# Kernel optimization log

Measured on AMD Instinct MI355X. Metric: run time of the kernel, lower is better.

The kernel has to match this reference:

```python
import jax, jax.numpy as jnp
import numpy as np
import math

PRE_D = 2048   # pre_d_model (scaled from 8192)
D = 4096       # d_model (scaled from 16384)
N = 64         # d_state (scaled from 128)
K = 4          # d_conv
EXP = 2
L = 128        # sequence_length
DI1 = EXP * PRE_D
DI2 = EXP * D
DTR1 = math.ceil(PRE_D / 16)
DTR2 = math.ceil(D / 16)


def _sinusoid(max_len, d):
    pe = np.zeros((max_len, d), np.float32)
    pos = np.arange(max_len, dtype=np.float32)[:, None]
    div = np.exp(np.arange(0, d, 2, dtype=np.float32) * (-math.log(10000.0) / d))
    pe[:, 0::2] = np.sin(pos * div)
    pe[:, 1::2] = np.cos(pos * div)
    return jnp.asarray(pe)


def _mamba_params(key, d_in, d_out, di, dtr, n, k):
    ks = jax.random.split(key, 6)
    s = 0.02
    dt = jnp.exp(jax.random.uniform(ks[4], (di,)) * (math.log(0.1) - math.log(1e-3)) + math.log(1e-3))
    return dict(
        in_proj=jax.random.normal(ks[0], (2 * di, d_in)) * s,
        conv_w=jax.random.normal(ks[1], (di, k)) * s,
        conv_b=jnp.zeros((di,)),
        x_proj=jax.random.normal(ks[2], (dtr + 2 * n, di)) * s,
        dt_w=jax.random.normal(ks[3], (di, dtr)) * s,
        dt_b=jnp.log(jnp.expm1(dt)),  # softplus^-1 of dt init
        A_log=jnp.log(jnp.tile(jnp.arange(1, n + 1, dtype=jnp.float32), (di, 1))),
        D=jnp.ones((di,)),
        out_proj=jax.random.normal(ks[5], (d_out, di)) * s,
    )


def setup_inputs() -> dict:
    key = jax.random.key(0)
    k1, k2, k3, k4 = jax.random.split(key, 4)
    inp = {
        'pe': _sinusoid(L, PRE_D),                              # (L, PRE_D)
        'to_cond_w': jax.random.normal(k3, (PRE_D, 1)) * 0.02,  # Linear(1 -> PRE_D)
        'to_cond_b': jnp.zeros((PRE_D,)),
        'condition': jax.random.normal(k4, (1,)),
        'batch': 1,
    }
    for pref, p in (('m1_', _mamba_params(k1, PRE_D, PRE_D, DI1, DTR1, N, K)),
                    ('m2_', _mamba_params(k2, PRE_D, D, DI2, DTR2, N, K))):
        for name, v in p.items():
            inp[pref + name] = v
    return inp


def _silu(x):
    return x * jax.nn.sigmoid(x)


def _mamba(x, in_w, cw, cb, xp_w, dt_w, dt_b, A_log, Dp, out_w, dtr, n):
    # x: (B, L, d_in)
    xz = x @ in_w.T                     # (B, L, 2*di)
    xr, z = jnp.split(xz, 2, axis=-1)
    kk = cw.shape[1]
    Lx = xr.shape[1]
    xpad = jnp.pad(xr, ((0, 0), (kk - 1, 0), (0, 0)))  # causal pad
    conv = sum(cw[:, i] * xpad[:, i:i + Lx, :] for i in range(kk)) + cb
    xr = _silu(conv)
    dbc = xr @ xp_w.T                   # (B, L, dtr + 2n)
    dt = dbc[..., :dtr]
    Bm = dbc[..., dtr:dtr + n]
    Cm = dbc[..., dtr + n:]
    dt = jax.nn.softplus(dt @ dt_w.T + dt_b)           # (B, L, di)
    A = -jnp.exp(A_log)                                 # (di, n)
    dA = jnp.exp(jnp.einsum('bld,dn->bldn', dt, A))
    dBx = jnp.einsum('bld,bln,bld->bldn', dt, Bm, xr)

    def comb(c1, c2):
        a1, b1 = c1
        a2, b2 = c2
        return a2 * a1, a2 * b1 + b2

    _, h = jax.lax.associative_scan(comb, (dA, dBx), axis=1)  # (B, L, di, n)
    y = jnp.einsum('bldn,bln->bld', h, Cm) + xr * Dp
    y = y * _silu(z)
    return y @ out_w.T


def reference(pe, to_cond_w, to_cond_b, condition,
              m1_in_proj, m1_conv_w, m1_conv_b, m1_x_proj, m1_dt_w, m1_dt_b, m1_A_log, m1_D, m1_out_proj,
              m2_in_proj, m2_conv_w, m2_conv_b, m2_x_proj, m2_dt_w, m2_dt_b, m2_A_log, m2_D, m2_out_proj,
              batch):
    cond = condition.reshape(-1, 1, 1)
    c = jnp.einsum('bli,oi->blo', cond, to_cond_w) + to_cond_b   # (Bc,1,PRE_D)
    x = jnp.tile(pe[None], (batch, 1, 1)) + c                    # (B, L, PRE_D)
    x = _mamba(x, m1_in_proj, m1_conv_w, m1_conv_b, m1_x_proj, m1_dt_w, m1_dt_b,
               m1_A_log, m1_D, m1_out_proj, DTR1, N)
    x = _mamba(x, m2_in_proj, m2_conv_w, m2_conv_b, m2_x_proj, m2_dt_w, m2_dt_b,
               m2_A_log, m2_D, m2_out_proj, DTR2, N)
    return x
```

## Files before the change

kernel.cpp:

```cpp
#include <hip/hip_runtime.h>
#include <hip/hip_bf16.h>
#include <math.h>


typedef __attribute__((ext_vector_type(8))) short short8_t;
typedef __attribute__((ext_vector_type(4))) float f32x4;

__device__ __forceinline__ float sigmoidf_(float x) {
  return 1.0f / (1.0f + __expf(-x));
}
__device__ __forceinline__ float softplusf_(float x) {
  return fmaxf(x, 0.0f) + log1pf(expf(-fabsf(x)));
}
__device__ __forceinline__ void splitbf(float f, ushort& h, ushort& lo) {
  __hip_bfloat16 hb = __float2bfloat16(f);
  h = *reinterpret_cast<ushort*>(&hb);
  float hf = __bfloat162float(hb);
  __hip_bfloat16 lb = __float2bfloat16(f - hf);
  lo = *reinterpret_cast<ushort*>(&lb);
}
__device__ __forceinline__ void tsplit(float f, ushort& h, ushort& lo) {
  unsigned u = __float_as_uint(f);
  h = (ushort)(u >> 16);
  float r = f - __uint_as_float(u & 0xFFFF0000u);
  lo = (ushort)(__float_as_uint(r) >> 16);
}
__device__ __forceinline__ size_t poff(int l, int d) {
  return (size_t)(d >> 5) * 8192 + (size_t)((d >> 3) & 3) * 1024 +
         (size_t)l * 8 + (d & 7);
}
__device__ __forceinline__ void g2l16(const float* g, float* lp) {
  __builtin_amdgcn_global_load_lds(
      (const __attribute__((address_space(1))) unsigned int*)g,
      (__attribute__((address_space(3))) unsigned int*)lp, 16, 0, 0);
}

__global__ __launch_bounds__(256) void k_prep(const float* __restrict__ pe,
                                              const float* __restrict__ cw,
                                              const float* __restrict__ cb,
                                              const float* __restrict__ cond,
                                              ushort* __restrict__ xp) {
  int i = blockIdx.x * 256 + threadIdx.x;
  int d = i & 2047;
  int l = i >> 11;
  float v = pe[i] + cond[0] * cw[d] + cb[d];
  ushort h, lo;
  splitbf(v, h, lo);
  size_t o = poff(l, d);
  xp[o] = h;
  xp[o + 4096] = lo;
}

#define KWS 32
__global__ __launch_bounds__(256, 4) void k_gemmW(const ushort* __restrict__ Ap,
                                                  const float* __restrict__ W, int ldw,
                                                  float* __restrict__ P,
                                                  int N, int Ks) {
  __shared__ float Wlds[2][4][32][32];

  const int n0   = blockIdx.x * 128;
  const int m0   = blockIdx.y * 64;
  const int s    = blockIdx.z;
  const int kbeg = s * Ks;
  const int t    = threadIdx.x;
  const int l    = t & 63;
  const int w    = t >> 6;
  const int lr   = l & 15;
  const int lg   = l >> 4;

  f32x4 acc[4][2];
#pragma unroll
  for (int mi = 0; mi < 4; ++mi)
#pragma unroll
    for (int ni = 0; ni < 2; ++ni) acc[mi][ni] = (f32x4)(0.0f);

  const int grow = l >> 3;
  const int gg   = (l & 7) ^ (grow & 7);
  const float* gW[4];
#pragma unroll
  for (int i = 0; i < 4; ++i)
    gW[i] = W + (size_t)(n0 + 32 * w + 8 * i + grow) * ldw + kbeg + gg * 4;

  const ushort* pA0 = Ap + (size_t)(kbeg >> 5) * 8192;
  const int nIter = Ks / KWS;
  const int j0 = (blockIdx.x * 3 + blockIdx.y * 5 + s) % nIter;

#pragma unroll
  for (int i = 0; i < 4; ++i)
    g2l16(gW[i] + (size_t)j0 * KWS, &Wlds[0][w][8 * i][0]);

  for (int j = 0; j < nIter; ++j) {
    const int bi = j & 1;
    const int cur = (j0 + j) % nIter;
    const bool more = (j + 1 < nIter);

    const ushort* pAj = pA0 + (size_t)cur * 8192;
    short8_t ah[4], al[4];
#pragma unroll
    for (int mi = 0; mi < 4; ++mi) {
      const size_t fo = (size_t)lg * 1024 + (size_t)(m0 + 16 * mi + lr) * 8;
      ah[mi] = *(const short8_t*)(pAj + fo);
      al[mi] = *(const short8_t*)(pAj + 4096 + fo);
    }
    __builtin_amdgcn_sched_barrier(0);
    if (more) {
      const int nxt = (j0 + j + 1) % nIter;
#pragma unroll
      for (int i = 0; i < 4; ++i)
        g2l16(gW[i] + (size_t)nxt * KWS, &Wlds[bi ^ 1][w][8 * i][0]);
      asm volatile("s_waitcnt vmcnt(4)" ::: "memory");
    } else {
      asm volatile("s_waitcnt vmcnt(0)" ::: "memory");
    }
    __builtin_amdgcn_sched_barrier(0);
    const float* Wb = &Wlds[bi][w][0][0];
#pragma unroll
    for (int ni = 0; ni < 2; ++ni) {
      const int r32 = 16 * ni + lr;
      const int rsw = r32 & 7;
      const float4 v0 = *(const float4*)(Wb + r32 * 32 + (((2 * lg) ^ rsw) * 4));
      const float4 v1 = *(const float4*)(Wb + r32 * 32 + (((2 * lg + 1) ^ rsw) * 4));
      short8_t bh, bl;
      {
        const float f8[8] = {v0.x, v0.y, v0.z, v0.w, v1.x, v1.y, v1.z, v1.w};
#pragma unroll
        for (int e = 0; e < 8; ++e) {
          ushort h, lo;
          tsplit(f8[e], h, lo);
          bh[e] = (short)h;
          bl[e] = (short)lo;
        }
      }
#pragma unroll
      for (int mi = 0; mi < 4; ++mi) {
        acc[mi][ni] = __builtin_amdgcn_mfma_f32_16x16x32_bf16(ah[mi], bh, acc[mi][ni], 0, 0, 0);
        acc[mi][ni] = __builtin_amdgcn_mfma_f32_16x16x32_bf16(al[mi], bh, acc[mi][ni], 0, 0, 0);
        acc[mi][ni] = __builtin_amdgcn_mfma_f32_16x16x32_bf16(ah[mi], bl, acc[mi][ni], 0, 0, 0);
      }
    }
  }

  float* Pd = P + (size_t)s * 128 * N + n0 + 32 * w;
#pragma unroll
  for (int mi = 0; mi < 4; ++mi)
#pragma unroll
    for (int ni = 0; ni < 2; ++ni) {
#pragma unroll
      for (int jj = 0; jj < 4; ++jj) {
        const int m = m0 + 16 * mi + 4 * lg + jj;
        Pd[(size_t)m * N + 16 * ni + lr] = acc[mi][ni][jj];
      }
    }
}

#define KSTEP 32
__global__ __launch_bounds__(256, 2) void k_gemm(const ushort* __restrict__ Ap,
                                                 const float* __restrict__ W, int ldw,
                                                 float* __restrict__ P,
                                                 int N, int Ks) {
  __shared__ ushort Ws[2][2][4][128][8];

  const int n0   = blockIdx.x * 128;
  const int s    = blockIdx.z;
  const int kbeg = s * Ks;
  const int t    = threadIdx.x;
  const int l    = t & 63;
  const int w    = t >> 6;
  const int wm   = w >> 1;
  const int wn   = w & 1;
  const int lr   = l & 15;
  const int lg   = l >> 4;

  f32x4 acc[4][4];
#pragma unroll
  for (int mi = 0; mi < 4; ++mi)
#pragma unroll
    for (int ni = 0; ni < 4; ++ni) acc[mi][ni] = (f32x4)(0.0f);

  const int srow = t >> 3;
  const int sk16 = t & 7;
  const int skb  = sk16 >> 1;
  const int se0  = (sk16 & 1) * 4;
  const float* pWg = W + (size_t)(n0 + srow) * ldw + kbeg + sk16 * 4;

  const ushort* pAc = Ap + (size_t)(kbeg >> 5) * 8192;
  const int arow = 64 * wm + lr;
  const int brow = 64 * wn + lr;

  const int nIter = Ks / KSTEP;
  float4 wv[4];

#pragma unroll
  for (int r = 0; r < 4; ++r)
    wv[r] = *(const float4*)(pWg + (size_t)(r * 32) * ldw);
#pragma unroll
  for (int r = 0; r < 4; ++r) {
    ushort4 h4, l4;
    splitbf(wv[r].x, h4.x, l4.x); splitbf(wv[r].y, h4.y, l4.y);
    splitbf(wv[r].z, h4.z, l4.z); splitbf(wv[r].w, h4.w, l4.w);
    *(ushort4*)&Ws[0][0][skb][srow + 32 * r][se0] = h4;
    *(ushort4*)&Ws[0][1][skb][srow + 32 * r][se0] = l4;
  }
  __syncthreads();

  for (int j = 0; j < nIter; ++j) {
    const int bi = j & 1;
    const bool more = (j + 1 < nIter);

    const ushort* pAj = pAc + (size_t)j * 8192;
    short8_t ah[4], al[4];
#pragma unroll
    for (int mi = 0; mi < 4; ++mi) {
      const size_t fo = (size_t)lg * 1024 + (size_t)(arow + 16 * mi) * 8;
      ah[mi] = *(const short8_t*)(pAj + fo);
      al[mi] = *(const short8_t*)(pAj + 4096 + fo);
    }
    if (more) {
      const size_t ko = (size_t)(j + 1) * KSTEP;
#pragma unroll
      for (int r = 0; r < 4; ++r)
        wv[r] = *(const float4*)(pWg + ko + (size_t)(r * 32) * ldw);
    }
    short8_t bh[4], bl[4];
#pragma unroll
    for (int ni = 0; ni < 4; ++ni) {
      bh[ni] = *(const short8_t*)&Ws[bi][0][lg][brow + 16 * ni][0];
      bl[ni] = *(const short8_t*)&Ws[bi][1][lg][brow + 16 * ni][0];
    }
#pragma unroll
    for (int mi = 0; mi < 4; ++mi)
#pragma unroll
      for (int ni = 0; ni < 4; ++ni) {
        acc[mi][ni] = __builtin_amdgcn_mfma_f32_16x16x32_bf16(ah[mi], bh[ni], acc[mi][ni], 0, 0, 0);
        acc[mi][ni] = __builtin_amdgcn_mfma_f32_16x16x32_bf16(al[mi], bh[ni], acc[mi][ni], 0, 0, 0);
        acc[mi][ni] = __builtin_amdgcn_mfma_f32_16x16x32_bf16(ah[mi], bl[ni], acc[mi][ni], 0, 0, 0);
      }
    if (more) {
#pragma unroll
      for (int r = 0; r < 4; ++r) {
        ushort4 h4, l4;
        splitbf(wv[r].x, h4.x, l4.x); splitbf(wv[r].y, h4.y, l4.y);
        splitbf(wv[r].z, h4.z, l4.z); splitbf(wv[r].w, h4.w, l4.w);
        *(ushort4*)&Ws[bi ^ 1][0][skb][srow + 32 * r][se0] = h4;
        *(ushort4*)&Ws[bi ^ 1][1][skb][srow + 32 * r][se0] = l4;
      }
    }
    __syncthreads();
  }

  float* Pd = P + (size_t)s * 128 * N + n0 + 64 * wn;
#pragma unroll
  for (int mi = 0; mi < 4; ++mi)
#pragma unroll
    for (int ni = 0; ni < 4; ++ni) {
#pragma unroll
      for (int jj = 0; jj < 4; ++jj) {
        const int m = 64 * wm + 16 * mi + 4 * lg + jj;
        Pd[(size_t)m * N + 16 * ni + lr] = acc[mi][ni][jj];
      }
    }
}

__global__ __launch_bounds__(256) void k_reduce(const float* __restrict__ P,
                                                float* __restrict__ Y,
                                                ushort* __restrict__ Yp,
                                                int MN, int N, int S, int ep,
                                                const float* __restrict__ bias) {
  int i = (blockIdx.x * 256 + threadIdx.x) * 4;
  if (i >= MN) return;
  float4 v = *(const float4*)&P[i];
  for (int s = 1; s < S; ++s) {
    float4 p = *(const float4*)&P[(size_t)s * MN + i];
    v.x += p.x; v.y += p.y; v.z += p.z; v.w += p.w;
  }
  int n = i % N;
  int l = i / N;
  if (ep & 1) {
    const float4 b = *(const float4*)&bias[n];
    v.x = softplusf_(v.x + b.x);
    v.y = softplusf_(v.y + b.y);
    v.z = softplusf_(v.z + b.z);
    v.w = softplusf_(v.w + b.w);
  }
  if (ep & 4) *(float4*)&Y[i] = v;
  if (ep & 2) {
    ushort4 h4, l4;
    splitbf(v.x, h4.x, l4.x);
    splitbf(v.y, h4.y, l4.y);
    splitbf(v.z, h4.z, l4.z);
    splitbf(v.w, h4.w, l4.w);
    size_t o = poff(l, n);
    *(ushort4*)&Yp[o] = h4;
    *(ushort4*)&Yp[o + 4096] = l4;
  }
}

__global__ __launch_bounds__(256) void k_reduceA(const float* __restrict__ P,
                                                 float* __restrict__ Y, int MN) {
  int g = blockIdx.y;
  int i = (blockIdx.x * 256 + threadIdx.x) * 4;
  if (i >= MN) return;
  const float* Pp = P + (size_t)g * 8 * MN;
  float4 v = *(const float4*)&Pp[i];
  for (int s = 1; s < 8; ++s) {
    float4 p = *(const float4*)&Pp[(size_t)s * MN + i];
    v.x += p.x; v.y += p.y; v.z += p.z; v.w += p.w;
  }
  *(float4*)&Y[(size_t)g * MN + i] = v;
}

__global__ __launch_bounds__(256) void k_conv_silu(const float* __restrict__ xz,
                                                   const float* __restrict__ cw,
                                                   const float* __restrict__ cb,
                                                   float* __restrict__ xc,
                                                   ushort* __restrict__ xcp,
                                                   int DI, int lg2DI) {
  int i = blockIdx.x * 256 + threadIdx.x;
  int l = i >> lg2DI;
  int d = i & (DI - 1);
  const float4 w = *(const float4*)&cw[d * 4];
  const float* xr = xz + d;
  int ld = 2 * DI;
  float s = cb[d];
  s += w.w * xr[l * ld];
  if (l >= 1) s += w.z * xr[(l - 1) * ld];
  if (l >= 2) s += w.y * xr[(l - 2) * ld];
  if (l >= 3) s += w.x * xr[(l - 3) * ld];
  float v = s * sigmoidf_(s);
  xc[i] = v;
  ushort h, lo;
  splitbf(v, h, lo);
  size_t o = poff(l, d);
  xcp[o] = h;
  xcp[o + 4096] = lo;
}

__global__ __launch_bounds__(256) void k_scan(const float* __restrict__ dt,
                                              const float* __restrict__ xc,
                                              const float* __restrict__ dbc,
                                              const float* __restrict__ A_log,
                                              const float* __restrict__ Dp,
                                              float* __restrict__ y,
                                              int DI, int DTR) {
  __shared__ float cs[4][32][65];
  const int wid = threadIdx.x >> 6;
  const int n   = threadIdx.x & 63;
  const int d   = blockIdx.x * 4 + wid;
  const int du  = __builtin_amdgcn_readfirstlane(d);
  const float A  = -__expf(A_log[(size_t)du * 64 + n]);
  const float Dd = Dp[du];
  const int ldbc = DTR + 128;
  const float* Bp = dbc + DTR + n;
  const float* Cp = dbc + DTR + 64 + n;
  float h = 0.0f;
  for (int l0 = 0; l0 < 128; l0 += 32) {
#pragma unroll 8
    for (int l = l0; l < l0 + 32; ++l) {
      float dtv = dt[(size_t)l * DI + du];
      float xcv = xc[(size_t)l * DI + du];
      float dA  = __expf(dtv * A);
      float bx  = dtv * xcv;
      h = fmaf(dA, h, bx * Bp[(size_t)l * ldbc]);
      cs[wid][l - l0][n] = h * Cp[(size_t)l * ldbc];
    }
    __syncthreads();
    const int r = n & 31, hf = n >> 5;
    float ssum = 0.0f;
#pragma unroll
    for (int j = 0; j < 32; ++j) ssum += cs[wid][r][hf * 32 + j];
    ssum += __shfl_xor(ssum, 32, 64);
    if (n < 32) {
      int ll = l0 + r;
      float xcv = xc[(size_t)ll * DI + du];
      y[(size_t)ll * DI + du] = ssum + xcv * Dd;
    }
    __syncthreads();
  }
}

__global__ __launch_bounds__(256) void k_gate(const float* __restrict__ yb,
                                              const float* __restrict__ xz,
                                              ushort* __restrict__ yp,
                                              int DI, int lg2DI) {
  int i = blockIdx.x * 256 + threadIdx.x;
  int l = i >> lg2DI;
  int d = i & (DI - 1);
  float z = xz[((size_t)l << (lg2DI + 1)) + DI + d];
  float v = yb[i] * (z * sigmoidf_(z));
  ushort h, lo;
  splitbf(v, h, lo);
  size_t o = poff(l, d);
  yp[o] = h;
  yp[o + 4096] = lo;
}

struct GemmCtx {
  float* part;
  float* part2;
  long long cap;
};

static inline void reduce_stage(float* dstF, ushort* dstP, int N, int S, int ep,
                                const float* bias, const GemmCtx& cx,
                                hipStream_t stream) {
  const int MN = 128 * N;
  const int rb = (MN / 4 + 255) / 256;
  if (S <= 16) {
    k_reduce<<<rb, 256, 0, stream>>>(cx.part, dstF, dstP, MN, N, S, ep, bias);
  } else {
    k_reduceA<<<dim3(rb, S / 8), 256, 0, stream>>>(cx.part, cx.part2, MN);
    k_reduce<<<rb, 256, 0, stream>>>(cx.part2, dstF, dstP, MN, N, S / 8, ep, bias);
  }
}

static inline void gemmS(const ushort* Ap, const float* W, int ldw,
                         float* dstF, ushort* dstP,
                         int N, int K, int Sdes, int ep,
                         const float* bias, const GemmCtx& cx, hipStream_t stream) {
  int S = Sdes;
  if (S > K / KSTEP) S = K / KSTEP;
  if (S < 1) S = 1;
  while (S > 1 && (long long)S * 128 * N > cx.cap) S >>= 1;
  const int Ks = K / S;
  const bool direct = (S == 1 && ep == 4);
  dim3 g(N / 128, 1, S);
  k_gemm<<<g, 256, 0, stream>>>(Ap, W, ldw, direct ? dstF : cx.part, N, Ks);
  if (!direct) reduce_stage(dstF, dstP, N, S, ep, bias, cx, stream);
}

static inline void gemmW(const ushort* Ap, const float* W, int ldw,
                         float* dstF, ushort* dstP,
                         int N, int K, int Sdes, int ep,
                         const float* bias, const GemmCtx& cx, hipStream_t stream) {
  int S = Sdes;
  if (S > K / KWS) S = K / KWS;
  if (S < 1) S = 1;
  while (S > 1 && (long long)S * 128 * N > cx.cap) S >>= 1;
  const int Ks = K / S;
  const bool direct = (S == 1 && ep == 4);
  dim3 g(N / 128, 2, S);
  k_gemmW<<<g, 256, 0, stream>>>(Ap, W, ldw, direct ? dstF : cx.part, N, Ks);
  if (!direct) reduce_stage(dstF, dstP, N, S, ep, bias, cx, stream);
}

extern "C" void kernel_launch(void* const* d_in, const int* in_sizes, int n_in,
                              void* d_out, int out_size, void* d_ws, size_t ws_size,
                              hipStream_t stream) {
  const float* pe        = (const float*)d_in[0];
  const float* to_cond_w = (const float*)d_in[1];
  const float* to_cond_b = (const float*)d_in[2];
  const float* condition = (const float*)d_in[3];
  const int o = (in_sizes[4] == 1) ? 5 : 4;
  const float* m1_in_proj  = (const float*)d_in[o + 0];
  const float* m1_conv_w   = (const float*)d_in[o + 1];
  const float* m1_conv_b   = (const float*)d_in[o + 2];
  const float* m1_x_proj   = (const float*)d_in[o + 3];
  const float* m1_dt_w     = (const float*)d_in[o + 4];
  const float* m1_dt_b     = (const float*)d_in[o + 5];
  const float* m1_A_log    = (const float*)d_in[o + 6];
  const float* m1_D        = (const float*)d_in[o + 7];
  const float* m1_out_proj = (const float*)d_in[o + 8];
  const float* m2_in_proj  = (const float*)d_in[o + 9];
  const float* m2_conv_w   = (const float*)d_in[o + 10];
  const float* m2_conv_b   = (const float*)d_in[o + 11];
  const float* m2_x_proj   = (const float*)d_in[o + 12];
  const float* m2_dt_w     = (const float*)d_in[o + 13];
  const float* m2_dt_b     = (const float*)d_in[o + 14];
  const float* m2_A_log    = (const float*)d_in[o + 15];
  const float* m2_D        = (const float*)d_in[o + 16];
  const float* m2_out_proj = (const float*)d_in[o + 17];

  float* ws = (float*)d_ws;
  float*  xz   = ws;
  float*  xc   = ws + 2097152;
  float*  dbc  = ws + 3145728;
  float*  dtb  = ws + 3194880;
  float*  yb   = ws + 4243456;
  ushort* x0p  = (ushort*)(ws + 5292032);
  ushort* xcp  = (ushort*)(ws + 5554176);
  ushort* dbcp = (ushort*)(ws + 6602752);
  ushort* ybp  = (ushort*)(ws + 6651904);
  ushort* midp = (ushort*)(ws + 7700480);
  float*  part2 = ws + 7962624;
  float*  part  = ws + 8749056;

  GemmCtx cx;
  cx.part = part;
  cx.part2 = part2;
  cx.cap = (long long)(ws_size / 4) - 8749056;
  if (cx.cap < 0) cx.cap = 0;

  k_prep<<<1024, 256, 0, stream>>>(pe, to_cond_w, to_cond_b, condition, x0p);

  gemmW(x0p, m1_in_proj, 2048, xz, nullptr, 8192, 2048, 8, 4, nullptr, cx, stream);
  k_conv_silu<<<(128 * 4096) / 256, 256, 0, stream>>>(xz, m1_conv_w, m1_conv_b,
                                                      xc, xcp, 4096, 12);
  gemmS(xcp, m1_x_proj, 4096, dbc, dbcp, 256, 4096, 128, 6, nullptr, cx, stream);
  gemmS(dbcp, m1_dt_w, 128, dtb, nullptr, 4096, 128, 4, 5, m1_dt_b, cx, stream);
  k_scan<<<1024, 256, 0, stream>>>(dtb, xc, dbc, m1_A_log, m1_D, yb, 4096, 128);
  k_gate<<<(128 * 4096) / 256, 256, 0, stream>>>(yb, xz, ybp, 4096, 12);
  gemmW(ybp, m1_out_proj, 4096, nullptr, midp, 2048, 4096, 16, 2, nullptr, cx, stream);

  gemmW(midp, m2_in_proj, 2048, xz, nullptr, 16384, 2048, 4, 4, nullptr, cx, stream);
  k_conv_silu<<<(128 * 8192) / 256, 256, 0, stream>>>(xz, m2_conv_w, m2_conv_b,
                                                      xc, xcp, 8192, 13);
  gemmS(xcp, m2_x_proj, 8192, dbc, dbcp, 384, 8192, 128, 6, nullptr, cx, stream);
  gemmS(dbcp, m2_dt_w, 256, dtb, nullptr, 8192, 256, 4, 5, m2_dt_b, cx, stream);
  k_scan<<<2048, 256, 0, stream>>>(dtb, xc, dbc, m2_A_log, m2_D, yb, 8192, 256);
  k_gate<<<(128 * 8192) / 256, 256, 0, stream>>>(yb, xz, ybp, 8192, 13);
  gemmW(ybp, m2_out_proj, 8192, (float*)d_out, nullptr, 4096, 8192, 8, 4, nullptr, cx, stream);
}
```

Before: 372.8 us.

## Widen gemmW tile to full M, triple-buffer W and double-buffer A registers

The weight-streaming GEMM kernel now handles all 128 rows per block instead of splitting M across two blocks. This halves redundant loads of the fp32 weight tile. The W tile moves from a double to a triple LDS buffer, A fragments are double-buffered in registers across an unrolled-by-two loop, and a fixed vmcnt(20) wait keeps more loads in flight. Split-K counts are doubled to keep the grid size similar. The cost is higher register pressure (launch bounds drop from 4 to 2 waves), and the loop now assumes an even iteration count.

```diff
diff --git a/kernel.cpp b/kernel.cpp
--- a/kernel.cpp
+++ b/kernel.cpp
@@ -52,14 +52,13 @@
 }
 
 #define KWS 32
-__global__ __launch_bounds__(256, 4) void k_gemmW(const ushort* __restrict__ Ap,
+__global__ __launch_bounds__(256, 2) void k_gemmW(const ushort* __restrict__ Ap,
                                                   const float* __restrict__ W, int ldw,
                                                   float* __restrict__ P,
                                                   int N, int Ks) {
-  __shared__ float Wlds[2][4][32][32];
+  __shared__ float Wlds[3][4][32][32];
 
   const int n0   = blockIdx.x * 128;
-  const int m0   = blockIdx.y * 64;
   const int s    = blockIdx.z;
   const int kbeg = s * Ks;
   const int t    = threadIdx.x;
@@ -68,9 +67,9 @@
   const int lr   = l & 15;
   const int lg   = l >> 4;
 
-  f32x4 acc[4][2];
-#pragma unroll
-  for (int mi = 0; mi < 4; ++mi)
+  f32x4 acc[8][2];
+#pragma unroll
+  for (int mi = 0; mi < 8; ++mi)
 #pragma unroll
     for (int ni = 0; ni < 2; ++ni) acc[mi][ni] = (f32x4)(0.0f);
 
@@ -83,71 +82,87 @@
 
   const ushort* pA0 = Ap + (size_t)(kbeg >> 5) * 8192;
   const int nIter = Ks / KWS;
-  const int j0 = (blockIdx.x * 3 + blockIdx.y * 5 + s) % nIter;
-
-#pragma unroll
-  for (int i = 0; i < 4; ++i)
-    g2l16(gW[i] + (size_t)j0 * KWS, &Wlds[0][w][8 * i][0]);
-
-  for (int j = 0; j < nIter; ++j) {
-    const int bi = j & 1;
-    const int cur = (j0 + j) % nIter;
-    const bool more = (j + 1 < nIter);
-
-    const ushort* pAj = pA0 + (size_t)cur * 8192;
-    short8_t ah[4], al[4];
-#pragma unroll
-    for (int mi = 0; mi < 4; ++mi) {
-      const size_t fo = (size_t)lg * 1024 + (size_t)(m0 + 16 * mi + lr) * 8;
-      ah[mi] = *(const short8_t*)(pAj + fo);
-      al[mi] = *(const short8_t*)(pAj + 4096 + fo);
-    }
+  const int j0 = (blockIdx.x * 3 + s) % nIter;
+
+  short8_t ahA[8], alA[8], ahB[8], alB[8];
+
+#define STAGE(POS)                                                          \
+  do {                                                                      \
+    const int c_ = (j0 + (POS)) % nIter;                                    \
+    float* d_ = &Wlds[(POS) % 3][w][0][0];                                  \
+    _Pragma("unroll") for (int i_ = 0; i_ < 4; ++i_)                        \
+      g2l16(gW[i_] + (size_t)c_ * KWS, d_ + 8 * i_ * 32);                   \
+  } while (0)
+#define LOADA(AH, AL, POS)                                                  \
+  do {                                                                      \
+    const ushort* p_ = pA0 + (size_t)((j0 + (POS)) % nIter) * 8192;         \
+    _Pragma("unroll") for (int mi_ = 0; mi_ < 8; ++mi_) {                   \
+      const size_t fo_ = (size_t)lg * 1024 + (size_t)(16 * mi_ + lr) * 8;   \
+      AH[mi_] = *(const short8_t*)(p_ + fo_);                               \
+      AL[mi_] = *(const short8_t*)(p_ + 4096 + fo_);                        \
+    }                                                                       \
+  } while (0)
+#define COMPUTE(AH, AL, POS)                                                \
+  do {                                                                      \
+    const float* Wb_ = &Wlds[(POS) % 3][w][0][0];                           \
+    _Pragma("unroll") for (int ni_ = 0; ni_ < 2; ++ni_) {                   \
+      const int r_ = 16 * ni_ + lr;                                         \
+      const int rsw_ = r_ & 7;                                              \
+      const float4 v0_ = *(const float4*)(Wb_ + r_ * 32 + (((2 * lg) ^ rsw_) * 4)); \
+      const float4 v1_ = *(const float4*)(Wb_ + r_ * 32 + (((2 * lg + 1) ^ rsw_) * 4)); \
+      short8_t bh_, bl_;                                                    \
+      {                                                                     \
+        const float f8_[8] = {v0_.x, v0_.y, v0_.z, v0_.w,                   \
+                              v1_.x, v1_.y, v1_.z, v1_.w};                  \
+        _Pragma("unroll") for (int e_ = 0; e_ < 8; ++e_) {                  \
+          ushort h_, lo_;                                                   \
+          tsplit(f8_[e_], h_, lo_);                                         \
+          bh_[e_] = (short)h_;                                              \
+          bl_[e_] = (short)lo_;                                             \
+        }                                                                   \
+      }                                                                     \
+      _Pragma("unroll") for (int mi_ = 0; mi_ < 8; ++mi_) {                 \
+        acc[mi_][ni_] = __builtin_amdgcn_mfma_f32_16x16x32_bf16(AH[mi_], bh_, acc[mi_][ni_], 0, 0, 0); \
+        acc[mi_][ni_] = __builtin_amdgcn_mfma_f32_16x16x32_bf16(AL[mi_], bh_, acc[mi_][ni_], 0, 0, 0); \
+        acc[mi_][ni_] = __builtin_amdgcn_mfma_f32_16x16x32_bf16(AH[mi_], bl_, acc[mi_][ni_], 0, 0, 0); \
+      }                                                                     \
+    }                                                                       \
+  } while (0)
+#define WAIT20                                                              \
+  do {                                                                      \
+    asm volatile("s_waitcnt vmcnt(20)" ::: "memory");                       \
+    __builtin_amdgcn_sched_barrier(0);                                      \
+  } while (0)
+
+  STAGE(0);
+  STAGE(1);
+  LOADA(ahA, alA, 0);
+
+  for (int j = 0; j < nIter; j += 2) {
+    LOADA(ahB, alB, j + 1);
     __builtin_amdgcn_sched_barrier(0);
-    if (more) {
-      const int nxt = (j0 + j + 1) % nIter;
-#pragma unroll
-      for (int i = 0; i < 4; ++i)
-        g2l16(gW[i] + (size_t)nxt * KWS, &Wlds[bi ^ 1][w][8 * i][0]);
-      asm volatile("s_waitcnt vmcnt(4)" ::: "memory");
-    } else {
-      asm volatile("s_waitcnt vmcnt(0)" ::: "memory");
-    }
+    STAGE(j + 2);
+    WAIT20;
+    COMPUTE(ahA, alA, j);
+    LOADA(ahA, alA, j + 2);
     __builtin_amdgcn_sched_barrier(0);
-    const float* Wb = &Wlds[bi][w][0][0];
+    STAGE(j + 3);
+    WAIT20;
+    COMPUTE(ahB, alB, j + 1);
+  }
+#undef STAGE
+#undef LOADA
+#undef COMPUTE
+#undef WAIT20
+
+  float* Pd = P + (size_t)s * 128 * N + n0 + 32 * w;
+#pragma unroll
+  for (int mi = 0; mi < 8; ++mi)
 #pragma unroll
     for (int ni = 0; ni < 2; ++ni) {
-      const int r32 = 16 * ni + lr;
-      const int rsw = r32 & 7;
-      const float4 v0 = *(const float4*)(Wb + r32 * 32 + (((2 * lg) ^ rsw) * 4));
-      const float4 v1 = *(const float4*)(Wb + r32 * 32 + (((2 * lg + 1) ^ rsw) * 4));
-      short8_t bh, bl;
-      {
-        const float f8[8] = {v0.x, v0.y, v0.z, v0.w, v1.x, v1.y, v1.z, v1.w};
-#pragma unroll
-        for (int e = 0; e < 8; ++e) {
-          ushort h, lo;
-          tsplit(f8[e], h, lo);
-          bh[e] = (short)h;
-          bl[e] = (short)lo;
-        }
-      }
-#pragma unroll
-      for (int mi = 0; mi < 4; ++mi) {
-        acc[mi][ni] = __builtin_amdgcn_mfma_f32_16x16x32_bf16(ah[mi], bh, acc[mi][ni], 0, 0, 0);
-        acc[mi][ni] = __builtin_amdgcn_mfma_f32_16x16x32_bf16(al[mi], bh, acc[mi][ni], 0, 0, 0);
-        acc[mi][ni] = __builtin_amdgcn_mfma_f32_16x16x32_bf16(ah[mi], bl, acc[mi][ni], 0, 0, 0);
-      }
-    }
-  }
-
-  float* Pd = P + (size_t)s * 128 * N + n0 + 32 * w;
-#pragma unroll
-  for (int mi = 0; mi < 4; ++mi)
-#pragma unroll
-    for (int ni = 0; ni < 2; ++ni) {
 #pragma unroll
       for (int jj = 0; jj < 4; ++jj) {
-        const int m = m0 + 16 * mi + 4 * lg + jj;
+        const int m = 16 * mi + 4 * lg + jj;
         Pd[(size_t)m * N + 16 * ni + lr] = acc[mi][ni][jj];
       }
     }
@@ -433,12 +448,12 @@
                          int N, int K, int Sdes, int ep,
                          const float* bias, const GemmCtx& cx, hipStream_t stream) {
   int S = Sdes;
-  if (S > K / KWS) S = K / KWS;
+  if (S > K / (2 * KWS)) S = K / (2 * KWS);
   if (S < 1) S = 1;
   while (S > 1 && (long long)S * 128 * N > cx.cap) S >>= 1;
   const int Ks = K / S;
   const bool direct = (S == 1 && ep == 4);
-  dim3 g(N / 128, 2, S);
+  dim3 g(N / 128, 1, S);
   k_gemmW<<<g, 256, 0, stream>>>(Ap, W, ldw, direct ? dstF : cx.part, N, Ks);
   if (!direct) reduce_stage(dstF, dstP, N, S, ep, bias, cx, stream);
 }
@@ -499,7 +514,7 @@
   gemmS(dbcp, m1_dt_w, 128, dtb, nullptr, 4096, 128, 4, 5, m1_dt_b, cx, stream);
   k_scan<<<1024, 256, 0, stream>>>(dtb, xc, dbc, m1_A_log, m1_D, yb, 4096, 128);
   k_gate<<<(128 * 4096) / 256, 256, 0, stream>>>(yb, xz, ybp, 4096, 12);
-  gemmW(ybp, m1_out_proj, 4096, nullptr, midp, 2048, 4096, 16, 2, nullptr, cx, stream);
+  gemmW(ybp, m1_out_proj, 4096, nullptr, midp, 2048, 4096, 32, 2, nullptr, cx, stream);
 
   gemmW(midp, m2_in_proj, 2048, xz, nullptr, 16384, 2048, 4, 4, nullptr, cx, stream);
   k_conv_silu<<<(128 * 8192) / 256, 256, 0, stream>>>(xz, m2_conv_w, m2_conv_b,
@@ -508,5 +523,5 @@
   gemmS(dbcp, m2_dt_w, 256, dtb, nullptr, 8192, 256, 4, 5, m2_dt_b, cx, stream);
   k_scan<<<2048, 256, 0, stream>>>(dtb, xc, dbc, m2_A_log, m2_D, yb, 8192, 256);
   k_gate<<<(128 * 8192) / 256, 256, 0, stream>>>(yb, xz, ybp, 8192, 13);
-  gemmW(ybp, m2_out_proj, 8192, (float*)d_out, nullptr, 4096, 8192, 8, 4, nullptr, cx, stream);
-}
+  gemmW(ybp, m2_out_proj, 8192, (float*)d_out, nullptr, 4096, 8192, 16, 4, nullptr, cx, stream);
+}
```

Result: no change. 373.4 us (+0.2%).
